# Kernel optimization log

Hardware: AMD Instinct MI355X
Metric: run time of the kernel (lower is better)

Reference implementation:

```python
import jax, jax.numpy as jnp
import numpy as np

B, T, I, H, L, O = 64, 2048, 14, 100, 10, 1


def setup_inputs() -> dict:
    key = jax.random.key(0)
    ks = jax.random.split(key, 8)
    s = 1.0 / np.sqrt(H)  # PyTorch RNN init scale: U(-1/sqrt(H), 1/sqrt(H))
    u = lambda k, shape: jax.random.uniform(k, shape, jnp.float32, -s, s)
    return dict(
        x=jax.random.normal(ks[0], (B, T, I), jnp.float32),
        hidden=jnp.zeros((L, B, H), jnp.float32),
        w_ih0=u(ks[1], (H, I)),        # layer 0 input weights
        w_ihL=u(ks[2], (L - 1, H, H)),  # layers 1..L-1 input weights
        w_hh=u(ks[3], (L, H, H)),
        b_ih=u(ks[4], (L, H)),
        b_hh=u(ks[5], (L, H)),
        fc_w=u(ks[6], (O, H)),
        fc_b=u(ks[7], (O,)),
    )


def reference(x, hidden, w_ih0, w_ihL, w_hh, b_ih, b_hh, fc_w, fc_b):
    # nn.RNN (tanh): h_t^l = tanh(x W_ih^T + b_ih + h_{t-1} W_hh^T + b_hh)
    def step(h, x_t):  # h: [L,B,H], x_t: [B,I]
        hs = []
        inp = x_t
        for l in range(L):
            w = w_ih0 if l == 0 else w_ihL[l - 1]
            h_l = jnp.tanh(inp @ w.T + b_ih[l] + h[l] @ w_hh[l].T + b_hh[l])
            hs.append(h_l)
            inp = h_l
        return jnp.stack(hs), inp  # carry new hidden, emit top-layer output

    h_final, outs = jax.lax.scan(step, hidden, jnp.swapaxes(x, 0, 1))  # outs: [T,B,H]
    flat = jnp.swapaxes(outs, 0, 1).reshape(-1, H)  # [B*T, H], matches view(-1, H)
    out = flat @ fc_w.T + fc_b  # [B*T, O]
    return out, h_final
```

## Files before the change

### kernel.cpp

```cpp
#include <hip/hip_runtime.h>

#define NL 10
#define NB 64
#define NT 2048
#define NI 14
#define NH 100
#define NS 4
#define BPS 16
#define CH 8
#define NTC (NT / CH)
#define HSTR 136
#define RC 104
#define PLANE (CH * BPS * RC)
#define NTHR 448
#define NW 7
#define FLAGW 16
#define FLAGBYTES 8192
#define ABORT_IDX (NL * NS * FLAGW)
#define SPIN_CAP (1 << 18)

typedef __attribute__((ext_vector_type(8))) short short8v;
typedef __attribute__((ext_vector_type(4))) float f32x4;

__device__ __forceinline__ unsigned ld_rlx(const unsigned* p) {
  return __hip_atomic_load(p, __ATOMIC_RELAXED, __HIP_MEMORY_SCOPE_AGENT);
}
__device__ __forceinline__ void st_rlx(unsigned* p, unsigned v) {
  __hip_atomic_store(p, v, __ATOMIC_RELAXED, __HIP_MEMORY_SCOPE_AGENT);
}
__device__ __forceinline__ unsigned short f2bf(float f) {
  unsigned u = __float_as_uint(f);
  return (unsigned short)((u + 0x7FFFu + ((u >> 16) & 1u)) >> 16);
}
__device__ __forceinline__ float bf2f(unsigned short u) {
  return __uint_as_float((unsigned)u << 16);
}
__device__ __forceinline__ float fast_tanh(float v) {
  float e = __expf(2.f * v);
  return 1.f - 2.f / (e + 1.f);
}

__device__ __forceinline__ short8v ld16_sys(const unsigned short* p) {
  short8v r;
  asm volatile("global_load_dwordx4 %0, %1, off sc0 sc1"
               : "=v"(r) : "v"(p) : "memory");
  return r;
}
__device__ __forceinline__ void st16_sys(unsigned short* p, short8v v) {
  asm volatile("global_store_dwordx4 %0, %1, off sc0 sc1"
               :: "v"(p), "v"(v) : "memory");
}

__device__ __forceinline__ int wait_ge(const unsigned* p, unsigned tgt,
                                       unsigned* abortf) {
  int iters = 0;
  while (ld_rlx(p) < tgt) {
    if (++iters > SPIN_CAP) { st_rlx(abortf, 1u); return 1; }
    if ((iters & 63) == 0 && ld_rlx(abortf) != 0) return 1;
    __builtin_amdgcn_s_sleep(2);
  }
  return 0;
}

__global__ void zero_flags(unsigned* p) {
  p[blockIdx.x * 256 + threadIdx.x] = 0u;
}

__global__ __launch_bounds__(NTHR, 2)
void rnn_mfma(const float* __restrict__ x, const float* __restrict__ hidden,
              const float* __restrict__ w_ih0, const float* __restrict__ w_ihL,
              const float* __restrict__ w_hh, const float* __restrict__ b_ih,
              const float* __restrict__ b_hh, const float* __restrict__ fc_w,
              const float* __restrict__ fc_b, float* __restrict__ out,
              float* __restrict__ hfin, unsigned* __restrict__ prog,
              unsigned short* __restrict__ ring, int D) {
  __shared__ unsigned short hHi[BPS][HSTR];
  __shared__ unsigned short hLo[BPS][HSTR];
  __shared__ float fcwL[112];
  __shared__ int sAbort;

  const int bid = blockIdx.x;
  const int l = bid / NS;
  const int s = bid - l * NS;
  const int tid = threadIdx.x;
  const int b0 = s * BPS;
  const int w = tid >> 6;
  const int ln = tid & 63;
  const int rowl = ln & 15;
  const int kg = (ln >> 4) & 3;

  for (int i = tid; i < BPS * HSTR; i += NTHR) {
    int r = i / HSTR, cc = i - r * HSTR;
    unsigned short hv = 0, lv = 0;
    if (cc < NH) {
      float f = hidden[(size_t)l * NB * NH + (size_t)(b0 + r) * NH + cc];
      hv = f2bf(f);
      lv = f2bf(f - bf2f(hv));
    }
    (&hHi[0][0])[i] = hv;
    (&hLo[0][0])[i] = lv;
  }
  for (int i = tid; i < 112; i += NTHR) fcwL[i] = (i < NH) ? fc_w[i] : 0.f;
  if (tid == 0) sAbort = 0;

  const int j = w * 16 + rowl;
  const float* Whh = w_hh + (size_t)l * NH * NH;
  const float* Wih = (l == 0) ? w_ih0 : (w_ihL + (size_t)(l - 1) * NH * NH);
  const int KI = (l == 0) ? NI : NH;

  short8v bhh[4], bih[4];
#pragma unroll
  for (int kc = 0; kc < 4; ++kc) {
    short8v f0 = {}, g0 = {};
    const int kb = kc * 32 + kg * 8;
    if (j < NH) {
#pragma unroll
      for (int e = 0; e < 8; ++e) {
        const int k = kb + e;
        if (k < NH) f0[e] = (short)f2bf(Whh[j * NH + k]);
        if (k < KI) g0[e] = (short)f2bf(Wih[j * KI + k]);
      }
    }
    bhh[kc] = f0; bih[kc] = g0;
  }
  const float bias = (j < NH) ? b_ih[l * NH + j] + b_hh[l * NH + j] : 0.f;
  const float fcb = fc_b[0];

  const unsigned* pin = prog + ((l > 0 ? (l - 1) * NS + s : 0)) * FLAGW;
  const unsigned* pout = prog + ((l < NL - 1 ? (l + 1) * NS + s : 0)) * FLAGW;
  unsigned* pme = prog + (l * NS + s) * FLAGW;
  unsigned* abortf = prog + ABORT_IDX;

  const unsigned short* rin =
      ring + (size_t)(l > 0 ? (l - 1) * NS + s : 0) * D * PLANE;
  unsigned short* rout = ring + (size_t)(l * NS + s) * D * PLANE;

  __syncthreads();

  for (int c = 0; c < NTC; ++c) {
    if (tid == 0) {
      int ab = 0;
      if (l > 0) ab |= wait_ge(pin, (unsigned)(c + 1), abortf);
      if (!ab && l < NL - 1 && c >= D)
        ab |= wait_ge(pout, (unsigned)(c - D + 1), abortf);
      sAbort = ab;
    }
    __syncthreads();
    if (sAbort) return;

    short8v xh[CH], xl[CH];
    if (l == 0 && w < NW) {
#pragma unroll
      for (int st = 0; st < CH; ++st) {
        short8v hh = {}, ll = {};
        const float* xp =
            x + (size_t)(b0 + rowl) * (NT * NI) + (size_t)(c * CH + st) * NI;
        if (kg < 2) {
#pragma unroll
          for (int e = 0; e < 8; ++e) {
            const int k = kg * 8 + e;
            if (k < NI) {
              float f = xp[k];
              unsigned short hu = f2bf(f);
              hh[e] = (short)hu;
              ll[e] = (short)f2bf(f - bf2f(hu));
            }
          }
        }
        xh[st] = hh; xl[st] = ll;
      }
    }

    const unsigned short* rbc = rin + (size_t)(c % D) * PLANE;
    unsigned short* robc = rout + (size_t)(c % D) * PLANE;

#pragma unroll
    for (int st = 0; st < CH; ++st) {
      const int t = c * CH + st;

      unsigned short nh[4], nl[4];
      if (w < NW) {
        short8v ic0, ic1, ic2, ic3;
        if (l > 0) {
          const unsigned short* rbase = rbc + (st * BPS + rowl) * RC + kg * 8;
          ic0 = ld16_sys(rbase + 0);
          ic1 = ld16_sys(rbase + 32);
          ic2 = ld16_sys(rbase + 64);
          ic3 = ld16_sys(rbase + 96);
        }

        short8v ahh[4], alo[4];
#pragma unroll
        for (int kc = 0; kc < 4; ++kc) {
          ahh[kc] = *(const short8v*)&hHi[rowl][kc * 32 + kg * 8];
          alo[kc] = *(const short8v*)&hLo[rowl][kc * 32 + kg * 8];
        }

        f32x4 acch = {0.f, 0.f, 0.f, 0.f};
        f32x4 accl = {0.f, 0.f, 0.f, 0.f};
#pragma unroll
        for (int kc = 0; kc < 4; ++kc) {
          acch = __builtin_amdgcn_mfma_f32_16x16x32_bf16(ahh[kc], bhh[kc], acch, 0, 0, 0);
          accl = __builtin_amdgcn_mfma_f32_16x16x32_bf16(alo[kc], bhh[kc], accl, 0, 0, 0);
        }

        f32x4 acci = {0.f, 0.f, 0.f, 0.f};
        if (l == 0) {
          acci = __builtin_amdgcn_mfma_f32_16x16x32_bf16(xh[st], bih[0], acci, 0, 0, 0);
          acci = __builtin_amdgcn_mfma_f32_16x16x32_bf16(xl[st], bih[0], acci, 0, 0, 0);
        } else {
          asm volatile("s_waitcnt vmcnt(0)" ::: "memory");
          __builtin_amdgcn_sched_barrier(0);
          acci = __builtin_amdgcn_mfma_f32_16x16x32_bf16(ic0, bih[0], acci, 0, 0, 0);
          acci = __builtin_amdgcn_mfma_f32_16x16x32_bf16(ic1, bih[1], acci, 0, 0, 0);
          acci = __builtin_amdgcn_mfma_f32_16x16x32_bf16(ic2, bih[2], acci, 0, 0, 0);
          acci = __builtin_amdgcn_mfma_f32_16x16x32_bf16(ic3, bih[3], acci, 0, 0, 0);
        }

#pragma unroll
        for (int r = 0; r < 4; ++r) {
          float v = fast_tanh(acch[r] + accl[r] + acci[r] + bias);
          nh[r] = f2bf(v);
          nl[r] = f2bf(v - bf2f(nh[r]));
        }
      }

      __syncthreads();

      if (w < NW && j < NH) {
#pragma unroll
        for (int r = 0; r < 4; ++r) {
          const int m = kg * 4 + r;
          hHi[m][j] = nh[r];
          hLo[m][j] = nl[r];
        }
      }
      __syncthreads();

      if (l < NL - 1) {
        if (tid < BPS * (RC / 8)) {
          const int rr = tid / 13, c8 = (tid - rr * 13) * 8;
          st16_sys(robc + (st * BPS + rr) * RC + c8,
                   *(const short8v*)&hHi[rr][c8]);
        }
      } else {
        if (tid < 256) {
          const int r = tid >> 4, ks = tid & 15;
          float sum = 0.f;
          for (int k = ks; k < NH; k += 16)
            sum = fmaf(bf2f(hHi[r][k]) + bf2f(hLo[r][k]), fcwL[k], sum);
          sum += __shfl_xor(sum, 1);
          sum += __shfl_xor(sum, 2);
          sum += __shfl_xor(sum, 4);
          sum += __shfl_xor(sum, 8);
          if (ks == 0) out[(size_t)(b0 + r) * NT + t] = sum + fcb;
        }
      }

      if (t == NT - 1) {
        for (int i = tid; i < BPS * NH; i += NTHR) {
          const int r = i / NH, jj = i - r * NH;
          hfin[(size_t)l * NB * NH + (size_t)(b0 + r) * NH + jj] =
              bf2f(hHi[r][jj]) + bf2f(hLo[r][jj]);
        }
      }
    }

    asm volatile("s_waitcnt vmcnt(0)" ::: "memory");
    __syncthreads();
    if (tid == 0) st_rlx(pme, (unsigned)(c + 1));
  }
}

extern "C" void kernel_launch(void* const* d_in, const int* in_sizes, int n_in,
                              void* d_out, int out_size, void* d_ws, size_t ws_size,
                              hipStream_t stream) {
  const float* x = (const float*)d_in[0];
  const float* hidden = (const float*)d_in[1];
  const float* w_ih0 = (const float*)d_in[2];
  const float* w_ihL = (const float*)d_in[3];
  const float* w_hh = (const float*)d_in[4];
  const float* b_ih = (const float*)d_in[5];
  const float* b_hh = (const float*)d_in[6];
  const float* fc_w = (const float*)d_in[7];
  const float* fc_b = (const float*)d_in[8];
  float* out = (float*)d_out;
  float* hfin = out + (size_t)NB * NT;
  unsigned* prog = (unsigned*)d_ws;
  unsigned short* ring = (unsigned short*)((char*)d_ws + FLAGBYTES);

  const size_t per_d = (size_t)(NL - 1) * NS * PLANE * 2;
  if (ws_size < FLAGBYTES + per_d + 128) return;
  int D = 32;
  while (D > 1 && FLAGBYTES + (size_t)D * per_d + 128 > ws_size) D >>= 1;

  zero_flags<<<8, 256, 0, stream>>>(prog);
  rnn_mfma<<<NL * NS, NTHR, 0, stream>>>(x, hidden, w_ih0, w_ihL, w_hh, b_ih,
                                         b_hh, fc_w, fc_b, out, hfin, prog,
                                         ring, D);
}
```

Before: 3.545 ms.

## Add producer warp with double-buffered hidden state and prefetched ring loads

New measurement: 3.265 ms. 7.9% less time.

```diff
diff --git a/kernel.cpp b/kernel.cpp
--- a/kernel.cpp
+++ b/kernel.cpp
@@ -9,10 +9,10 @@
 #define BPS 16
 #define CH 8
 #define NTC (NT / CH)
-#define HSTR 136
+#define HSTR 144
 #define RC 104
 #define PLANE (CH * BPS * RC)
-#define NTHR 448
+#define NTHR 512
 #define NW 7
 #define FLAGW 16
 #define FLAGBYTES 8192
@@ -40,15 +40,13 @@
   return 1.f - 2.f / (e + 1.f);
 }
 
-__device__ __forceinline__ short8v ld16_sys(const unsigned short* p) {
+__device__ __forceinline__ short8v ld16_dev(const unsigned short* p) {
   short8v r;
-  asm volatile("global_load_dwordx4 %0, %1, off sc0 sc1"
-               : "=v"(r) : "v"(p) : "memory");
+  asm volatile("global_load_dwordx4 %0, %1, off sc1" : "=v"(r) : "v"(p));
   return r;
 }
-__device__ __forceinline__ void st16_sys(unsigned short* p, short8v v) {
-  asm volatile("global_store_dwordx4 %0, %1, off sc0 sc1"
-               :: "v"(p), "v"(v) : "memory");
+__device__ __forceinline__ void st16_dev(unsigned short* p, short8v v) {
+  asm volatile("global_store_dwordx4 %0, %1, off sc1" :: "v"(p), "v"(v) : "memory");
 }
 
 __device__ __forceinline__ int wait_ge(const unsigned* p, unsigned tgt,
@@ -74,10 +72,11 @@
               const float* __restrict__ fc_b, float* __restrict__ out,
               float* __restrict__ hfin, unsigned* __restrict__ prog,
               unsigned short* __restrict__ ring, int D) {
-  __shared__ unsigned short hHi[BPS][HSTR];
-  __shared__ unsigned short hLo[BPS][HSTR];
-  __shared__ float fcwL[112];
+  __shared__ unsigned short hHi[2][BPS][HSTR];
+  __shared__ unsigned short hLo[2][BPS][HSTR];
+  __shared__ float fcwL[128];
   __shared__ int sAbort;
+  __shared__ int sReadyC;
 
   const int bid = blockIdx.x;
   const int l = bid / NS;
@@ -89,19 +88,20 @@
   const int rowl = ln & 15;
   const int kg = (ln >> 4) & 3;
 
-  for (int i = tid; i < BPS * HSTR; i += NTHR) {
-    int r = i / HSTR, cc = i - r * HSTR;
+  for (int i = tid; i < 2 * BPS * HSTR; i += NTHR) {
+    const int buf = i / (BPS * HSTR), rem = i - buf * (BPS * HSTR);
+    const int r = rem / HSTR, cc = rem - r * HSTR;
     unsigned short hv = 0, lv = 0;
-    if (cc < NH) {
+    if (buf == 0 && cc < NH) {
       float f = hidden[(size_t)l * NB * NH + (size_t)(b0 + r) * NH + cc];
       hv = f2bf(f);
       lv = f2bf(f - bf2f(hv));
     }
-    (&hHi[0][0])[i] = hv;
-    (&hLo[0][0])[i] = lv;
-  }
-  for (int i = tid; i < 112; i += NTHR) fcwL[i] = (i < NH) ? fc_w[i] : 0.f;
-  if (tid == 0) sAbort = 0;
+    (&hHi[0][0][0])[i] = hv;
+    (&hLo[0][0][0])[i] = lv;
+  }
+  for (int i = tid; i < 128; i += NTHR) fcwL[i] = (i < NH) ? fc_w[i] : 0.f;
+  if (tid == 0) { sAbort = 0; sReadyC = -1; }
 
   const int j = w * 16 + rowl;
   const float* Whh = w_hh + (size_t)l * NH * NH;
@@ -137,16 +137,26 @@
 
   __syncthreads();
 
+  float fcreg[32];
+  if (w == NW && l == NL - 1) {
+    const int q = ln & 3;
+#pragma unroll
+    for (int k = 0; k < 32; ++k) fcreg[k] = fcwL[q * 32 + k];
+  }
+
+  if (tid == 0) {
+    int ab = 0;
+    if (l > 0) ab = wait_ge(pin, 1u, abortf);
+    if (ab) sAbort = 1; else sReadyC = 0;
+  }
+  __syncthreads();
+  if (sAbort) return;
+
+  bool ready = false;
+
   for (int c = 0; c < NTC; ++c) {
-    if (tid == 0) {
-      int ab = 0;
-      if (l > 0) ab |= wait_ge(pin, (unsigned)(c + 1), abortf);
-      if (!ab && l < NL - 1 && c >= D)
-        ab |= wait_ge(pout, (unsigned)(c - D + 1), abortf);
-      sAbort = ab;
-    }
-    __syncthreads();
-    if (sAbort) return;
+    const unsigned short* rbc = rin + (size_t)(c % D) * PLANE;
+    unsigned short* robc = rout + (size_t)(c % D) * PLANE;
 
     short8v xh[CH], xl[CH];
     if (l == 0 && w < NW) {
@@ -171,29 +181,37 @@
       }
     }
 
-    const unsigned short* rbc = rin + (size_t)(c % D) * PLANE;
-    unsigned short* robc = rout + (size_t)(c % D) * PLANE;
+    short8v icA0, icA1, icA2, icA3, icB0, icB1, icB2, icB3;
 
 #pragma unroll
     for (int st = 0; st < CH; ++st) {
-      const int t = c * CH + st;
-
-      unsigned short nh[4], nl[4];
       if (w < NW) {
-        short8v ic0, ic1, ic2, ic3;
         if (l > 0) {
-          const unsigned short* rbase = rbc + (st * BPS + rowl) * RC + kg * 8;
-          ic0 = ld16_sys(rbase + 0);
-          ic1 = ld16_sys(rbase + 32);
-          ic2 = ld16_sys(rbase + 64);
-          ic3 = ld16_sys(rbase + 96);
-        }
-
+          if (st == 0) {
+            const unsigned short* r0 = rbc + (0 * BPS + rowl) * RC + kg * 8;
+            icA0 = ld16_dev(r0 + 0);  icA1 = ld16_dev(r0 + 32);
+            icA2 = ld16_dev(r0 + 64); icA3 = ld16_dev(r0 + 96);
+            const unsigned short* r1 = rbc + (1 * BPS + rowl) * RC + kg * 8;
+            icB0 = ld16_dev(r1 + 0);  icB1 = ld16_dev(r1 + 32);
+            icB2 = ld16_dev(r1 + 64); icB3 = ld16_dev(r1 + 96);
+          } else if (st < CH - 1) {
+            const unsigned short* rn = rbc + ((st + 1) * BPS + rowl) * RC + kg * 8;
+            if (st & 1) {
+              icA0 = ld16_dev(rn + 0);  icA1 = ld16_dev(rn + 32);
+              icA2 = ld16_dev(rn + 64); icA3 = ld16_dev(rn + 96);
+            } else {
+              icB0 = ld16_dev(rn + 0);  icB1 = ld16_dev(rn + 32);
+              icB2 = ld16_dev(rn + 64); icB3 = ld16_dev(rn + 96);
+            }
+          }
+        }
+
+        const int rb = st & 1;
         short8v ahh[4], alo[4];
 #pragma unroll
         for (int kc = 0; kc < 4; ++kc) {
-          ahh[kc] = *(const short8v*)&hHi[rowl][kc * 32 + kg * 8];
-          alo[kc] = *(const short8v*)&hLo[rowl][kc * 32 + kg * 8];
+          ahh[kc] = *(const short8v*)&hHi[rb][rowl][kc * 32 + kg * 8];
+          alo[kc] = *(const short8v*)&hLo[rb][rowl][kc * 32 + kg * 8];
         }
 
         f32x4 acch = {0.f, 0.f, 0.f, 0.f};
@@ -209,66 +227,120 @@
           acci = __builtin_amdgcn_mfma_f32_16x16x32_bf16(xh[st], bih[0], acci, 0, 0, 0);
           acci = __builtin_amdgcn_mfma_f32_16x16x32_bf16(xl[st], bih[0], acci, 0, 0, 0);
         } else {
-          asm volatile("s_waitcnt vmcnt(0)" ::: "memory");
+          if (st == CH - 1) asm volatile("s_waitcnt vmcnt(0)" ::: "memory");
+          else              asm volatile("s_waitcnt vmcnt(4)" ::: "memory");
           __builtin_amdgcn_sched_barrier(0);
-          acci = __builtin_amdgcn_mfma_f32_16x16x32_bf16(ic0, bih[0], acci, 0, 0, 0);
-          acci = __builtin_amdgcn_mfma_f32_16x16x32_bf16(ic1, bih[1], acci, 0, 0, 0);
-          acci = __builtin_amdgcn_mfma_f32_16x16x32_bf16(ic2, bih[2], acci, 0, 0, 0);
-          acci = __builtin_amdgcn_mfma_f32_16x16x32_bf16(ic3, bih[3], acci, 0, 0, 0);
-        }
-
+          if (st & 1) {
+            acci = __builtin_amdgcn_mfma_f32_16x16x32_bf16(icB0, bih[0], acci, 0, 0, 0);
+            acci = __builtin_amdgcn_mfma_f32_16x16x32_bf16(icB1, bih[1], acci, 0, 0, 0);
+            acci = __builtin_amdgcn_mfma_f32_16x16x32_bf16(icB2, bih[2], acci, 0, 0, 0);
+            acci = __builtin_amdgcn_mfma_f32_16x16x32_bf16(icB3, bih[3], acci, 0, 0, 0);
+          } else {
+            acci = __builtin_amdgcn_mfma_f32_16x16x32_bf16(icA0, bih[0], acci, 0, 0, 0);
+            acci = __builtin_amdgcn_mfma_f32_16x16x32_bf16(icA1, bih[1], acci, 0, 0, 0);
+            acci = __builtin_amdgcn_mfma_f32_16x16x32_bf16(icA2, bih[2], acci, 0, 0, 0);
+            acci = __builtin_amdgcn_mfma_f32_16x16x32_bf16(icA3, bih[3], acci, 0, 0, 0);
+          }
+        }
+
+        unsigned short nh[4], nl[4];
 #pragma unroll
         for (int r = 0; r < 4; ++r) {
           float v = fast_tanh(acch[r] + accl[r] + acci[r] + bias);
           nh[r] = f2bf(v);
           nl[r] = f2bf(v - bf2f(nh[r]));
         }
-      }
-
+        if (j < NH) {
+#pragma unroll
+          for (int r = 0; r < 4; ++r) {
+            const int m = kg * 4 + r;
+            hHi[rb ^ 1][m][j] = nh[r];
+            hLo[rb ^ 1][m][j] = nl[r];
+          }
+        }
+      } else {
+        if (st >= 1) {
+          const int b = st & 1;
+          if (l < NL - 1) {
+            for (int idx = ln; idx < BPS * (RC / 8); idx += 64) {
+              const int rr = idx / 13, c8 = (idx - rr * 13) * 8;
+              st16_dev(robc + ((st - 1) * BPS + rr) * RC + c8,
+                       *(const short8v*)&hHi[b][rr][c8]);
+            }
+          } else {
+            const int row = ln >> 2, q = ln & 3;
+            float sum = 0.f;
+#pragma unroll
+            for (int e = 0; e < 4; ++e) {
+              short8v hv = *(const short8v*)&hHi[b][row][q * 32 + e * 8];
+              short8v lv = *(const short8v*)&hLo[b][row][q * 32 + e * 8];
+#pragma unroll
+              for (int u = 0; u < 8; ++u)
+                sum = fmaf(bf2f((unsigned short)hv[u]) + bf2f((unsigned short)lv[u]),
+                           fcreg[e * 8 + u], sum);
+            }
+            sum += __shfl_xor(sum, 1);
+            sum += __shfl_xor(sum, 2);
+            if (q == 0)
+              out[(size_t)(b0 + row) * NT + (c * CH + st - 1)] = sum + fcb;
+          }
+        }
+        if (!ready && c + 1 < NTC && ln == 0) {
+          const bool okin = (l == 0) || (ld_rlx(pin) >= (unsigned)(c + 2));
+          const bool okout = (l == NL - 1) || (c + 1 < D) ||
+                             (ld_rlx(pout) >= (unsigned)(c + 2 - D));
+          if (okin && okout) { sReadyC = c + 1; ready = true; }
+        }
+      }
+
+      if (st == CH - 1 && tid == 0 && c + 1 < NTC) {
+        if (sReadyC < c + 1) {
+          int ab = 0;
+          if (l > 0) ab = wait_ge(pin, (unsigned)(c + 2), abortf);
+          if (!ab && l < NL - 1 && c + 1 >= D)
+            ab = wait_ge(pout, (unsigned)(c + 2 - D), abortf);
+          if (ab) sAbort = 1; else sReadyC = c + 1;
+        }
+      }
       __syncthreads();
-
-      if (w < NW && j < NH) {
-#pragma unroll
-        for (int r = 0; r < 4; ++r) {
-          const int m = kg * 4 + r;
-          hHi[m][j] = nh[r];
-          hLo[m][j] = nl[r];
-        }
-      }
-      __syncthreads();
-
+    }
+
+    if (sAbort) return;
+
+    if (w == NW) {
       if (l < NL - 1) {
-        if (tid < BPS * (RC / 8)) {
-          const int rr = tid / 13, c8 = (tid - rr * 13) * 8;
-          st16_sys(robc + (st * BPS + rr) * RC + c8,
-                   *(const short8v*)&hHi[rr][c8]);
+        for (int idx = ln; idx < BPS * (RC / 8); idx += 64) {
+          const int rr = idx / 13, c8 = (idx - rr * 13) * 8;
+          st16_dev(robc + ((CH - 1) * BPS + rr) * RC + c8,
+                   *(const short8v*)&hHi[0][rr][c8]);
         }
       } else {
-        if (tid < 256) {
-          const int r = tid >> 4, ks = tid & 15;
-          float sum = 0.f;
-          for (int k = ks; k < NH; k += 16)
-            sum = fmaf(bf2f(hHi[r][k]) + bf2f(hLo[r][k]), fcwL[k], sum);
-          sum += __shfl_xor(sum, 1);
-          sum += __shfl_xor(sum, 2);
-          sum += __shfl_xor(sum, 4);
-          sum += __shfl_xor(sum, 8);
-          if (ks == 0) out[(size_t)(b0 + r) * NT + t] = sum + fcb;
-        }
-      }
-
-      if (t == NT - 1) {
-        for (int i = tid; i < BPS * NH; i += NTHR) {
-          const int r = i / NH, jj = i - r * NH;
-          hfin[(size_t)l * NB * NH + (size_t)(b0 + r) * NH + jj] =
-              bf2f(hHi[r][jj]) + bf2f(hLo[r][jj]);
-        }
-      }
-    }
-
-    asm volatile("s_waitcnt vmcnt(0)" ::: "memory");
-    __syncthreads();
-    if (tid == 0) st_rlx(pme, (unsigned)(c + 1));
+        const int row = ln >> 2, q = ln & 3;
+        float sum = 0.f;
+#pragma unroll
+        for (int e = 0; e < 4; ++e) {
+          short8v hv = *(const short8v*)&hHi[0][row][q * 32 + e * 8];
+          short8v lv = *(const short8v*)&hLo[0][row][q * 32 + e * 8];
+#pragma unroll
+          for (int u = 0; u < 8; ++u)
+            sum = fmaf(bf2f((unsigned short)hv[u]) + bf2f((unsigned short)lv[u]),
+                       fcreg[e * 8 + u], sum);
+        }
+        sum += __shfl_xor(sum, 1);
+        sum += __shfl_xor(sum, 2);
+        if (q == 0)
+          out[(size_t)(b0 + row) * NT + (c * CH + CH - 1)] = sum + fcb;
+      }
+      asm volatile("s_waitcnt vmcnt(0)" ::: "memory");
+      if (ln == 0) st_rlx(pme, (unsigned)(c + 1));
+      ready = false;
+    }
+  }
+
+  for (int i = tid; i < BPS * NH; i += NTHR) {
+    const int r = i / NH, jj = i - r * NH;
+    hfin[(size_t)l * NB * NH + (size_t)(b0 + r) * NH + jj] =
+        bf2f(hHi[0][r][jj]) + bf2f(hLo[0][r][jj]);
   }
 }
 
```
